# Performance work log

Hardware: AMD Instinct MI355X
Metric: run time of the kernel (lower is better)

## Reference

```python
import jax, jax.numpy as jnp
import numpy as np

B, N, T, H = 16, 256, 96, 128
EPS = 1e-5


def setup_inputs() -> dict:
    key = jax.random.key(0)
    ks = jax.random.split(key, 9)
    return {
        "x": jax.random.normal(ks[0], (B, N, T), dtype=jnp.float32),
        "Wp": jax.random.normal(ks[1], (T, H), dtype=jnp.float32) / np.sqrt(T),
        "bp": jax.random.normal(ks[2], (H,), dtype=jnp.float32) * 0.01,
        "Wf": jax.random.normal(ks[3], (3 * H, H), dtype=jnp.float32) / np.sqrt(3 * H),
        "bf": jax.random.normal(ks[4], (H,), dtype=jnp.float32) * 0.01,
        "gamma": jnp.ones((H,), dtype=jnp.float32),
        "beta": jnp.zeros((H,), dtype=jnp.float32),
        "node_emb": jax.random.normal(ks[5], (N, H), dtype=jnp.float32),
        "time_emb": jax.random.normal(ks[6], (T, H), dtype=jnp.float32),
    }


def reference(x, Wp, bp, Wf, bf, gamma, beta, node_emb, time_emb):
    # input projection: [B,N,T] @ [T,H] -> [B,N,H]
    proj = jnp.einsum("bnt,th->bnh", x, Wp) + bp
    # Decompose the Linear over the concat [proj | node_pos | time_pos]:
    # cat(...) @ Wf == proj@W1 + node@W2 + time@W3  (same math, no huge concat)
    W1, W2, W3 = Wf[:H], Wf[H:2 * H], Wf[2 * H:]
    pre = (jnp.einsum("bnh,hk->bnk", proj, W1)[:, :, None, :]      # [B,N,1,H]
           + jnp.einsum("nh,hk->nk", node_emb, W2)[None, :, None, :]  # [1,N,1,H]
           + jnp.einsum("th,hk->tk", time_emb, W3)[None, None, :, :]  # [1,1,T,H]
           + bf)
    h = jax.nn.relu(pre)  # [B,N,T,H]
    mean = jnp.mean(h, axis=-1, keepdims=True)
    var = jnp.mean(jnp.square(h - mean), axis=-1, keepdims=True)
    return (h - mean) * jax.lax.rsqrt(var + EPS) * gamma + beta
```

## Files before the change

### kernel.cpp

```cpp
#include <hip/hip_runtime.h>
#include <hip/hip_bf16.h>

#define Bn 16
#define Nn 256
#define Tn 96
#define Hn 128
#define EPSf 1e-5f

typedef float vfloat4 __attribute__((ext_vector_type(4)));

__global__ __launch_bounds__(128) void precompute_kernel(
    const float* __restrict__ Wp, const float* __restrict__ bp,
    const float* __restrict__ Wf, const float* __restrict__ bf,
    const float* __restrict__ node_emb, const float* __restrict__ time_emb,
    float* __restrict__ M, float* __restrict__ E, float* __restrict__ Ct) {
  __shared__ float row[Hn];
  const int k = threadIdx.x;
  const int bid = blockIdx.x;
  if (bid < Tn) {
    const int t = bid;
    row[k] = Wp[t * Hn + k];
    __syncthreads();
    float acc = 0.f;
#pragma unroll 8
    for (int h = 0; h < Hn; ++h) acc = fmaf(row[h], Wf[h * Hn + k], acc);
    M[t * Hn + k] = acc;
  } else if (bid < Tn + Nn) {
    const int n = bid - Tn;
    row[k] = node_emb[n * Hn + k];
    __syncthreads();
    float acc = 0.f;
#pragma unroll 8
    for (int h = 0; h < Hn; ++h) acc = fmaf(row[h], Wf[(Hn + h) * Hn + k], acc);
    __syncthreads();
    row[k] = bp[k];
    __syncthreads();
#pragma unroll 8
    for (int h = 0; h < Hn; ++h) acc = fmaf(row[h], Wf[h * Hn + k], acc);
    E[n * Hn + k] = acc;
  } else {
    const int t = bid - Tn - Nn;
    row[k] = time_emb[t * Hn + k];
    __syncthreads();
    float acc = bf[k];
#pragma unroll 8
    for (int h = 0; h < Hn; ++h) acc = fmaf(row[h], Wf[(2 * Hn + h) * Hn + k], acc);
    Ct[t * Hn + k] = acc;
  }
}

__device__ __forceinline__ float swz_xor1(float v) {
  return __int_as_float(__builtin_amdgcn_ds_swizzle(__float_as_int(v), 0x041F));
}
__device__ __forceinline__ float swz_xor2(float v) {
  return __int_as_float(__builtin_amdgcn_ds_swizzle(__float_as_int(v), 0x081F));
}
__device__ __forceinline__ float swz_xor4(float v) {
  return __int_as_float(__builtin_amdgcn_ds_swizzle(__float_as_int(v), 0x101F));
}
__device__ __forceinline__ float swz_xor8(float v) {
  return __int_as_float(__builtin_amdgcn_ds_swizzle(__float_as_int(v), 0x201F));
}

__global__ __launch_bounds__(256) void main_kernel(
    const float* __restrict__ x, const float* __restrict__ M,
    const float* __restrict__ E, const float* __restrict__ Ct,
    const float* __restrict__ gamma, const float* __restrict__ beta,
    float* __restrict__ out) {
  const int bn = blockIdx.x;
  const int n = bn & (Nn - 1);
  __shared__ float xs[Tn];
  __shared__ __align__(16) float as[Hn];
  const int tid = threadIdx.x;

  if (tid < Tn) xs[tid] = x[bn * Tn + tid];
  __syncthreads();
  if (tid < Hn) {
    float acc = E[n * Hn + tid];
#pragma unroll 8
    for (int t = 0; t < Tn; ++t) acc = fmaf(xs[t], M[t * Hn + tid], acc);
    as[tid] = acc;
  }
  __syncthreads();

  const int wave = tid >> 6;
  const int lane = tid & 63;
  const int r  = lane >> 4;
  const int cg = lane & 15;
  const int c0i = 4 * cg;
  const int c1i = 64 + 4 * cg;

  const float4 a0 = *(const float4*)&as[c0i];
  const float4 a1 = *(const float4*)&as[c1i];
  const float4 g0 = *(const float4*)&gamma[c0i];
  const float4 g1 = *(const float4*)&gamma[c1i];
  const float4 q0 = *(const float4*)&beta[c0i];
  const float4 q1 = *(const float4*)&beta[c1i];
  const float inv128 = 1.f / 128.f;

#pragma unroll
  for (int i = 0; i < Tn / 16; ++i) {
    const int t = i * 16 + wave * 4 + r;
    const float4 c0 = *(const float4*)&Ct[t * Hn + c0i];
    const float4 c1 = *(const float4*)&Ct[t * Hn + c1i];
    const float h0 = fmaxf(a0.x + c0.x, 0.f);
    const float h1 = fmaxf(a0.y + c0.y, 0.f);
    const float h2 = fmaxf(a0.z + c0.z, 0.f);
    const float h3 = fmaxf(a0.w + c0.w, 0.f);
    const float h4 = fmaxf(a1.x + c1.x, 0.f);
    const float h5 = fmaxf(a1.y + c1.y, 0.f);
    const float h6 = fmaxf(a1.z + c1.z, 0.f);
    const float h7 = fmaxf(a1.w + c1.w, 0.f);

    float s = ((h0 + h1) + (h2 + h3)) + ((h4 + h5) + (h6 + h7));
    float ss = h0 * h0;
    ss = fmaf(h1, h1, ss); ss = fmaf(h2, h2, ss); ss = fmaf(h3, h3, ss);
    ss = fmaf(h4, h4, ss); ss = fmaf(h5, h5, ss); ss = fmaf(h6, h6, ss);
    ss = fmaf(h7, h7, ss);

    s += swz_xor1(s);  ss += swz_xor1(ss);
    s += swz_xor2(s);  ss += swz_xor2(ss);
    s += swz_xor4(s);  ss += swz_xor4(ss);
    s += swz_xor8(s);  ss += swz_xor8(ss);

    const float mean = s * inv128;
    const float var  = fmaf(-mean, mean, ss * inv128);
    const float inv  = rsqrtf(var + EPSf);

    vfloat4 o0, o1;
    o0.x = fmaf((h0 - mean) * inv, g0.x, q0.x);
    o0.y = fmaf((h1 - mean) * inv, g0.y, q0.y);
    o0.z = fmaf((h2 - mean) * inv, g0.z, q0.z);
    o0.w = fmaf((h3 - mean) * inv, g0.w, q0.w);
    o1.x = fmaf((h4 - mean) * inv, g1.x, q1.x);
    o1.y = fmaf((h5 - mean) * inv, g1.y, q1.y);
    o1.z = fmaf((h6 - mean) * inv, g1.z, q1.z);
    o1.w = fmaf((h7 - mean) * inv, g1.w, q1.w);

    float* rowp = &out[((size_t)bn * Tn + t) * Hn];
    __builtin_nontemporal_store(o0, (vfloat4*)(rowp + c0i));
    __builtin_nontemporal_store(o1, (vfloat4*)(rowp + c1i));
  }
}

extern "C" void kernel_launch(void* const* d_in, const int* in_sizes, int n_in,
                              void* d_out, int out_size, void* d_ws, size_t ws_size,
                              hipStream_t stream) {
  const float* x        = (const float*)d_in[0];
  const float* Wp       = (const float*)d_in[1];
  const float* bp       = (const float*)d_in[2];
  const float* Wf       = (const float*)d_in[3];
  const float* bf       = (const float*)d_in[4];
  const float* gamma    = (const float*)d_in[5];
  const float* beta     = (const float*)d_in[6];
  const float* node_emb = (const float*)d_in[7];
  const float* time_emb = (const float*)d_in[8];
  float* out = (float*)d_out;

  float* ws = (float*)d_ws;
  float* M  = ws;
  float* E  = ws + Tn * Hn;
  float* Ct = ws + Tn * Hn + Nn * Hn;

  precompute_kernel<<<Tn + Nn + Tn, 128, 0, stream>>>(Wp, bp, Wf, bf, node_emb,
                                                      time_emb, M, E, Ct);
  main_kernel<<<Bn * Nn, 256, 0, stream>>>(x, M, E, Ct, gamma, beta, out);
}
```

Measured before the change: 236.3 us.

## Split per-row projection into separate kernel from streaming LayerNorm writer

Moves the per-(b,n) projection GEMV, x·M+E, out of the streaming output kernel into its own kernel that writes an intermediate A buffer to workspace. The streaming kernel then only reads A, Ct, gamma and beta and writes the large normalized output, with no shared-memory GEMV or block barriers before its stores. This is meant to stop the 96-step serial dot-product from delaying each block's output writes. In exchange it adds a kernel launch and a round trip of A through global memory.

```diff
diff --git a/kernel.cpp b/kernel.cpp
--- a/kernel.cpp
+++ b/kernel.cpp
@@ -49,6 +49,21 @@
   }
 }
 
+__global__ __launch_bounds__(128) void abuild_kernel(
+    const float* __restrict__ x, const float* __restrict__ M,
+    const float* __restrict__ E, float* __restrict__ A) {
+  const int bn = blockIdx.x;
+  const int n = bn & (Nn - 1);
+  const int k = threadIdx.x;
+  __shared__ float xs[Tn];
+  if (k < Tn) xs[k] = x[bn * Tn + k];
+  __syncthreads();
+  float acc = E[n * Hn + k];
+#pragma unroll 8
+  for (int t = 0; t < Tn; ++t) acc = fmaf(xs[t], M[t * Hn + k], acc);
+  A[bn * Hn + k] = acc;
+}
+
 __device__ __forceinline__ float swz_xor1(float v) {
   return __int_as_float(__builtin_amdgcn_ds_swizzle(__float_as_int(v), 0x041F));
 }
@@ -62,27 +77,12 @@
   return __int_as_float(__builtin_amdgcn_ds_swizzle(__float_as_int(v), 0x201F));
 }
 
-__global__ __launch_bounds__(256) void main_kernel(
-    const float* __restrict__ x, const float* __restrict__ M,
-    const float* __restrict__ E, const float* __restrict__ Ct,
+__global__ __launch_bounds__(256) void stream_kernel(
+    const float* __restrict__ A, const float* __restrict__ Ct,
     const float* __restrict__ gamma, const float* __restrict__ beta,
     float* __restrict__ out) {
   const int bn = blockIdx.x;
-  const int n = bn & (Nn - 1);
-  __shared__ float xs[Tn];
-  __shared__ __align__(16) float as[Hn];
   const int tid = threadIdx.x;
-
-  if (tid < Tn) xs[tid] = x[bn * Tn + tid];
-  __syncthreads();
-  if (tid < Hn) {
-    float acc = E[n * Hn + tid];
-#pragma unroll 8
-    for (int t = 0; t < Tn; ++t) acc = fmaf(xs[t], M[t * Hn + tid], acc);
-    as[tid] = acc;
-  }
-  __syncthreads();
-
   const int wave = tid >> 6;
   const int lane = tid & 63;
   const int r  = lane >> 4;
@@ -90,8 +90,8 @@
   const int c0i = 4 * cg;
   const int c1i = 64 + 4 * cg;
 
-  const float4 a0 = *(const float4*)&as[c0i];
-  const float4 a1 = *(const float4*)&as[c1i];
+  const float4 a0 = *(const float4*)&A[bn * Hn + c0i];
+  const float4 a1 = *(const float4*)&A[bn * Hn + c1i];
   const float4 g0 = *(const float4*)&gamma[c0i];
   const float4 g1 = *(const float4*)&gamma[c1i];
   const float4 q0 = *(const float4*)&beta[c0i];
@@ -159,10 +159,12 @@
 
   float* ws = (float*)d_ws;
   float* M  = ws;
-  float* E  = ws + Tn * Hn;
-  float* Ct = ws + Tn * Hn + Nn * Hn;
+  float* E  = M + Tn * Hn;
+  float* Ct = E + Nn * Hn;
+  float* A  = Ct + Tn * Hn;
 
   precompute_kernel<<<Tn + Nn + Tn, 128, 0, stream>>>(Wp, bp, Wf, bf, node_emb,
                                                       time_emb, M, E, Ct);
-  main_kernel<<<Bn * Nn, 256, 0, stream>>>(x, M, E, Ct, gamma, beta, out);
+  abuild_kernel<<<Bn * Nn, 128, 0, stream>>>(x, M, E, A);
+  stream_kernel<<<Bn * Nn, 256, 0, stream>>>(A, Ct, gamma, beta, out);
 }
```

Result: no change. 238.3 us (+0.9%).
